# Kernel tuning notes

Measured on AMD Instinct MI355X. Metric: run time of the kernel, lower is better.

Reference implementation:

```python
import jax, jax.numpy as jnp
import numpy as np

E, K = 8, 2              # n_routed_experts, num_experts_per_tok
H, I = 2048, 1408        # hidden_size, moe_intermediate_size
IS = 2 * I               # shared experts intermediate (n_shared_experts * I)
B, S = 2, 512


def setup_inputs() -> dict:
    key = jax.random.key(0)
    ks = jax.random.split(key, 8)
    w = 0.02
    return {
        "hidden_states": jax.random.normal(ks[0], (B, S, H), jnp.float32),
        "router_w": jax.random.normal(ks[1], (E, H), jnp.float32) * w,
        "w_gate": jax.random.normal(ks[2], (E, I, H), jnp.float32) * w,
        "w_up": jax.random.normal(ks[3], (E, I, H), jnp.float32) * w,
        "w_down": jax.random.normal(ks[4], (E, H, I), jnp.float32) * w,
        "sw_gate": jax.random.normal(ks[5], (IS, H), jnp.float32) * w,
        "sw_up": jax.random.normal(ks[6], (IS, H), jnp.float32) * w,
        "sw_down": jax.random.normal(ks[7], (H, IS), jnp.float32) * w,
    }


def reference(hidden_states, router_w, w_gate, w_up, w_down, sw_gate, sw_up, sw_down):
    b, s, h = hidden_states.shape
    x = hidden_states.reshape(-1, h)                      # [T, H]
    t = x.shape[0]

    # Router: F.linear(x, gate_weight) -> softmax (fp32) -> topk (sorted)
    router_logits = x @ router_w.T                        # [T, E]
    scores = jax.nn.softmax(router_logits.astype(jnp.float32), axis=-1)
    routing_weights, selected = jax.lax.top_k(scores, K)  # [T, K]
    routing_weights = routing_weights / (routing_weights.sum(-1, keepdims=True) + 1e-6)
    routing_weights = routing_weights.astype(x.dtype)

    # Combine weights: [T, E], zero where expert not selected (exact gather/scatter math)
    cw = jnp.zeros((t, E), x.dtype).at[jnp.arange(t)[:, None], selected].add(routing_weights)

    # Per-expert SwiGLU FFN, batched over experts (grouped GEMM form)
    g = jnp.einsum('td,eid->eti', x, w_gate)              # [E, T, I]
    u = jnp.einsum('td,eid->eti', x, w_up)                # [E, T, I]
    y = jnp.einsum('eti,edi->etd', jax.nn.silu(g) * u, w_down)  # [E, T, H]
    moe_out = jnp.einsum('etd,te->td', y, cw)             # weighted combine -> [T, H]

    # Shared experts SwiGLU over all tokens
    shared = (jax.nn.silu(x @ sw_gate.T) * (x @ sw_up.T)) @ sw_down.T  # [T, H]

    final = (moe_out + shared).reshape(b, s, h)
    return final, router_logits
```

## Files before the change

### kernel.cpp

```cpp
#include <hip/hip_runtime.h>
#include <hip/hip_bf16.h>
#include <math.h>

#define T_TOK 1024
#define HDIM  2048
#define NEXP  8
#define IDIM  1408
#define ISH   2816
#define ROW_CAP 3072
#define ROWS_ALL 4096
#define MOE_TILES 24
#define NT_TOT 32

typedef __attribute__((ext_vector_type(8))) short bf16x8;
typedef __attribute__((ext_vector_type(4))) float f32x4;

static __device__ __forceinline__ unsigned short f2bf(float f) {
  __hip_bfloat16 h = __float2bfloat16(f);
  return __builtin_bit_cast(unsigned short, h);
}

__global__ __launch_bounds__(256) void router_kernel(
    const float* __restrict__ x, const float* __restrict__ rw,
    float* __restrict__ logits_out, int* __restrict__ selk, float* __restrict__ cwk)
{
  int t = blockIdx.x;
  int tid = threadIdx.x;
  float part[NEXP];
  const float* xr = x + (size_t)t * HDIM + tid * 8;
  float4 xa = *reinterpret_cast<const float4*>(xr);
  float4 xb = *reinterpret_cast<const float4*>(xr + 4);
  for (int e = 0; e < NEXP; ++e) {
    const float* wp = rw + (size_t)e * HDIM + tid * 8;
    float4 wa = *reinterpret_cast<const float4*>(wp);
    float4 wb = *reinterpret_cast<const float4*>(wp + 4);
    part[e] = xa.x*wa.x + xa.y*wa.y + xa.z*wa.z + xa.w*wa.w
            + xb.x*wb.x + xb.y*wb.y + xb.z*wb.z + xb.w*wb.w;
  }
  for (int e = 0; e < NEXP; ++e)
    for (int off = 32; off; off >>= 1)
      part[e] += __shfl_xor(part[e], off, 64);
  __shared__ float sums[4][NEXP];
  int wid = tid >> 6, lane = tid & 63;
  if (lane == 0) for (int e = 0; e < NEXP; ++e) sums[wid][e] = part[e];
  __syncthreads();
  if (tid == 0) {
    float lg[NEXP];
    for (int e = 0; e < NEXP; ++e) lg[e] = sums[0][e] + sums[1][e] + sums[2][e] + sums[3][e];
    float mx = lg[0];
    for (int e = 1; e < NEXP; ++e) mx = fmaxf(mx, lg[e]);
    float p[NEXP], s = 0.f;
    for (int e = 0; e < NEXP; ++e) { p[e] = expf(lg[e] - mx); s += p[e]; }
    for (int e = 0; e < NEXP; ++e) p[e] /= s;
    int i1 = 0;
    for (int e = 1; e < NEXP; ++e) if (lg[e] > lg[i1]) i1 = e;
    int i2 = -1;
    for (int e = 0; e < NEXP; ++e) { if (e == i1) continue; if (i2 < 0 || lg[e] > lg[i2]) i2 = e; }
    float denom = p[i1] + p[i2] + 1e-6f;
    selk[t*2] = i1; selk[t*2+1] = i2;
    cwk[t*2] = p[i1] / denom; cwk[t*2+1] = p[i2] / denom;
    for (int e = 0; e < NEXP; ++e) logits_out[t * NEXP + e] = lg[e];
  }
}

__global__ __launch_bounds__(512) void plan_kernel(
    const int* __restrict__ selk, const float* __restrict__ cwk,
    int* __restrict__ rowidx, int* __restrict__ tok_of_row,
    float* __restrict__ rowwgt, int* __restrict__ tile_tab)
{
  __shared__ int cnt[NEXP];
  __shared__ int seg[NEXP];
  int tid = threadIdx.x;
  int w = tid >> 6, lane = tid & 63;
  for (int i = tid; i < ROW_CAP; i += 512) { tok_of_row[i] = -1; rowwgt[i] = 0.f; }
  for (int i = tid; i < T_TOK; i += 512) { tok_of_row[ROW_CAP + i] = i; rowwgt[ROW_CAP + i] = 1.f; }
  int total = 0;
  for (int base = 0; base < 2 * T_TOK; base += 64) {
    unsigned long long m = __ballot(selk[base + lane] == w);
    total += __popcll(m);
  }
  if (lane == 0) cnt[w] = total;
  __syncthreads();
  if (tid == 0) {
    int s = 0;
    for (int e = 0; e < NEXP; ++e) { seg[e] = s; s += (cnt[e] + 127) & ~127; }
  }
  __syncthreads();
  int run = seg[w];
  for (int base = 0; base < 2 * T_TOK; base += 64) {
    int i = base + lane;
    bool f = selk[i] == w;
    unsigned long long m = __ballot(f);
    if (f) {
      int r = run + __popcll(m & ((1ull << lane) - 1ull));
      rowidx[i] = r;
      tok_of_row[r] = i >> 1;
      rowwgt[r] = cwk[i];
    }
    run += __popcll(m);
  }
  __syncthreads();
  if (tid < NT_TOT) {
    int e = -1, valid = 0;
    if (tid < MOE_TILES) {
      int base = tid * 128;
      for (int k = 0; k < NEXP; ++k) {
        int s0 = seg[k], s1 = s0 + ((cnt[k] + 127) & ~127);
        if (base >= s0 && base < s1) {
          e = k;
          valid = cnt[k] - (base - s0);
          if (valid > 128) valid = 128;
          if (valid < 0) valid = 0;
        }
      }
    } else { e = 0; valid = 128; }
    tile_tab[tid*2] = e;
    tile_tab[tid*2+1] = valid;
  }
}

__global__ __launch_bounds__(256) void gather_kernel(
    const float* __restrict__ x, const int* __restrict__ tok_of_row,
    unsigned short* __restrict__ xg)
{
  int r = blockIdx.x;
  int tid = threadIdx.x;
  int tok = tok_of_row[r];
  unsigned short* dst = xg + (size_t)r * HDIM + tid * 8;
  union { unsigned short us[8]; uint4 q; } p;
  if (tok < 0) {
    p.q = uint4{0, 0, 0, 0};
  } else {
    const float* src = x + (size_t)tok * HDIM + tid * 8;
    float4 a = *reinterpret_cast<const float4*>(src);
    float4 b = *reinterpret_cast<const float4*>(src + 4);
    p.us[0]=f2bf(a.x); p.us[1]=f2bf(a.y); p.us[2]=f2bf(a.z); p.us[3]=f2bf(a.w);
    p.us[4]=f2bf(b.x); p.us[5]=f2bf(b.y); p.us[6]=f2bf(b.z); p.us[7]=f2bf(b.w);
  }
  *reinterpret_cast<uint4*>(dst) = p.q;
}

__global__ __launch_bounds__(256) void wcvt_kernel(
    const float* __restrict__ s0, const float* __restrict__ s1,
    const float* __restrict__ s2, const float* __restrict__ s3,
    unsigned short* __restrict__ d0, unsigned short* __restrict__ d1,
    unsigned short* __restrict__ d2, unsigned short* __restrict__ d3,
    int b0, int b1, int b2)
{
  int b = blockIdx.x;
  const float* s; unsigned short* d; int off;
  if (b < b0)      { s = s0; d = d0; off = b; }
  else if (b < b1) { s = s1; d = d1; off = b - b0; }
  else if (b < b2) { s = s2; d = d2; off = b - b1; }
  else             { s = s3; d = d3; off = b - b2; }
  size_t idx = (size_t)off * 2048 + threadIdx.x * 8;
  float4 va = *reinterpret_cast<const float4*>(s + idx);
  float4 vb = *reinterpret_cast<const float4*>(s + idx + 4);
  union { unsigned short us[8]; uint4 q; } p;
  p.us[0]=f2bf(va.x); p.us[1]=f2bf(va.y); p.us[2]=f2bf(va.z); p.us[3]=f2bf(va.w);
  p.us[4]=f2bf(vb.x); p.us[5]=f2bf(vb.y); p.us[6]=f2bf(vb.z); p.us[7]=f2bf(vb.w);
  *reinterpret_cast<uint4*>(d + idx) = p.q;
}

static __device__ __forceinline__ void stage_t(
    const unsigned short* __restrict__ base, size_t ld, int k0,
    unsigned short* Ls, int wid, int lane)
{
  #pragma unroll
  for (int j = 0; j < 2; ++j) {
    int row = j * 64 + wid * 8 + (lane >> 3);
    int col = ((lane & 7) ^ (row & 7)) << 3;
    const unsigned short* src = base + (size_t)row * ld + k0 + col;
    unsigned short* dst = &Ls[(j * 64 + wid * 8) * 64];
    __builtin_amdgcn_global_load_lds(
        (const __attribute__((address_space(1))) void*)src,
        (__attribute__((address_space(3))) void*)dst, 16, 0, 0);
  }
}

__global__ __launch_bounds__(512) void gu_kernel(
    const unsigned short* __restrict__ xg,
    const unsigned short* __restrict__ wgb, const unsigned short* __restrict__ wub,
    const unsigned short* __restrict__ swgb, const unsigned short* __restrict__ swub,
    const float* __restrict__ rowwgt, const int* __restrict__ tile_tab,
    unsigned short* __restrict__ hg, unsigned short* __restrict__ hsh)
{
  int bid = blockIdx.x;
  int lb = (bid & 7) * 55 + (bid >> 3);
  int mt, nt;
  if (lb < MOE_TILES * 11) { mt = lb % MOE_TILES; nt = lb / MOE_TILES; }
  else { int s = lb - MOE_TILES * 11; mt = MOE_TILES + (s & 7); nt = s >> 3; }

  int e = tile_tab[mt*2], valid = tile_tab[mt*2+1];
  if (valid <= 0) return;
  bool sh = mt >= MOE_TILES;
  int m0 = mt * 128, n0 = nt * 128;
  const unsigned short *wg, *wu; unsigned short* hout; int ldo;
  if (sh) { wg = swgb; wu = swub; hout = hsh + (size_t)(m0 - ROW_CAP) * ISH; ldo = ISH; }
  else {
    size_t wo = (size_t)e * IDIM * HDIM;
    wg = wgb + wo; wu = wub + wo;
    hout = hg + (size_t)m0 * IDIM; ldo = IDIM;
  }

  __shared__ unsigned short As[128 * 64];
  __shared__ unsigned short Bg[128 * 64];
  __shared__ unsigned short Bu[128 * 64];

  int tid = threadIdx.x, wid = tid >> 6, lane = tid & 63;
  int wr = wid >> 2, wc = wid & 3;
  int fr = lane & 15, fq = lane >> 4, fq8 = fq << 3;

  f32x4 accg[4][2] = {{}};
  f32x4 accu[4][2] = {{}};

  const unsigned short* abase = xg + (size_t)m0 * HDIM;
  const unsigned short* gb = wg + (size_t)n0 * HDIM;
  const unsigned short* ub = wu + (size_t)n0 * HDIM;

  for (int k0 = 0; k0 < HDIM; k0 += 64) {
    stage_t(abase, HDIM, k0, As, wid, lane);
    stage_t(gb,    HDIM, k0, Bg, wid, lane);
    stage_t(ub,    HDIM, k0, Bu, wid, lane);
    __syncthreads();
    #pragma unroll
    for (int kk = 0; kk < 64; kk += 32) {
      bf16x8 a[4], bg[2], bu[2];
      #pragma unroll
      for (int m = 0; m < 4; ++m) {
        int row = wr * 64 + m * 16 + fr;
        a[m] = *reinterpret_cast<const bf16x8*>(&As[row * 64 + ((kk + fq8) ^ ((row & 7) << 3))]);
      }
      #pragma unroll
      for (int n = 0; n < 2; ++n) {
        int brow = wc * 32 + n * 16 + fr;
        int boff = brow * 64 + ((kk + fq8) ^ ((brow & 7) << 3));
        bg[n] = *reinterpret_cast<const bf16x8*>(&Bg[boff]);
        bu[n] = *reinterpret_cast<const bf16x8*>(&Bu[boff]);
      }
      #pragma unroll
      for (int m = 0; m < 4; ++m)
        #pragma unroll
        for (int n = 0; n < 2; ++n) {
          accg[m][n] = __builtin_amdgcn_mfma_f32_16x16x32_bf16(a[m], bg[n], accg[m][n], 0, 0, 0);
          accu[m][n] = __builtin_amdgcn_mfma_f32_16x16x32_bf16(a[m], bu[n], accu[m][n], 0, 0, 0);
        }
    }
    __syncthreads();
  }

  #pragma unroll
  for (int m = 0; m < 4; ++m)
    #pragma unroll
    for (int j = 0; j < 4; ++j) {
      int grow = wr * 64 + m * 16 + fq * 4 + j;
      float wv = rowwgt[m0 + grow];
      #pragma unroll
      for (int n = 0; n < 2; ++n) {
        float g = accg[m][n][j], u = accu[m][n][j];
        float hv = g / (1.f + __expf(-g)) * u * wv;
        hout[(size_t)grow * ldo + n0 + wc * 32 + n * 16 + fr] = f2bf(hv);
      }
    }
}

__global__ __launch_bounds__(512) void dn_kernel(
    const unsigned short* __restrict__ hg, const unsigned short* __restrict__ hsh,
    const unsigned short* __restrict__ wdb, const unsigned short* __restrict__ swdb,
    const int* __restrict__ tile_tab,
    float* __restrict__ ydn, float* __restrict__ outf)
{
  int bid = blockIdx.x;
  int lb = (bid & 7) * 64 + (bid >> 3);
  int mt, nt;
  if (lb < MOE_TILES * 16) { mt = lb % MOE_TILES; nt = lb / MOE_TILES; }
  else { int s = lb - MOE_TILES * 16; mt = MOE_TILES + (s & 7); nt = s >> 3; }

  int e = tile_tab[mt*2], valid = tile_tab[mt*2+1];
  if (valid <= 0) return;
  bool sh = mt >= MOE_TILES;
  int m0 = mt * 128, n0 = nt * 128;
  const unsigned short* abase; const unsigned short* bbase; int K; float* obase;
  if (sh) { abase = hsh + (size_t)(m0 - ROW_CAP) * ISH; K = ISH; bbase = swdb; obase = outf + (size_t)(m0 - ROW_CAP) * HDIM; }
  else { abase = hg + (size_t)m0 * IDIM; K = IDIM; bbase = wdb + (size_t)e * HDIM * IDIM; obase = ydn + (size_t)m0 * HDIM; }

  __shared__ unsigned short As[128 * 64];
  __shared__ unsigned short Bs[128 * 64];

  int tid = threadIdx.x, wid = tid >> 6, lane = tid & 63;
  int wr = wid >> 2, wc = wid & 3;
  int fr = lane & 15, fq = lane >> 4, fq8 = fq << 3;

  f32x4 acc[4][2] = {{}};

  const unsigned short* bb = bbase + (size_t)n0 * K;

  for (int k0 = 0; k0 < K; k0 += 64) {
    stage_t(abase, K, k0, As, wid, lane);
    stage_t(bb,    K, k0, Bs, wid, lane);
    __syncthreads();
    #pragma unroll
    for (int kk = 0; kk < 64; kk += 32) {
      bf16x8 a[4], b[2];
      #pragma unroll
      for (int m = 0; m < 4; ++m) {
        int row = wr * 64 + m * 16 + fr;
        a[m] = *reinterpret_cast<const bf16x8*>(&As[row * 64 + ((kk + fq8) ^ ((row & 7) << 3))]);
      }
      #pragma unroll
      for (int n = 0; n < 2; ++n) {
        int brow = wc * 32 + n * 16 + fr;
        b[n] = *reinterpret_cast<const bf16x8*>(&Bs[brow * 64 + ((kk + fq8) ^ ((brow & 7) << 3))]);
      }
      #pragma unroll
      for (int m = 0; m < 4; ++m)
        #pragma unroll
        for (int n = 0; n < 2; ++n)
          acc[m][n] = __builtin_amdgcn_mfma_f32_16x16x32_bf16(a[m], b[n], acc[m][n], 0, 0, 0);
    }
    __syncthreads();
  }
  #pragma unroll
  for (int m = 0; m < 4; ++m)
    #pragma unroll
    for (int j = 0; j < 4; ++j) {
      int grow = wr * 64 + m * 16 + fq * 4 + j;
      #pragma unroll
      for (int n = 0; n < 2; ++n)
        obase[(size_t)grow * HDIM + n0 + wc * 32 + n * 16 + fr] = acc[m][n][j];
    }
}

__global__ __launch_bounds__(256) void combine_kernel(
    const float* __restrict__ ydn, const int* __restrict__ rowidx,
    float* __restrict__ outf)
{
  int t = blockIdx.x;
  int c = threadIdx.x * 8;
  int r0 = rowidx[t*2], r1 = rowidx[t*2+1];
  const float4* a0 = reinterpret_cast<const float4*>(ydn + (size_t)r0 * HDIM + c);
  const float4* a1 = reinterpret_cast<const float4*>(ydn + (size_t)r1 * HDIM + c);
  float4* o = reinterpret_cast<float4*>(outf + (size_t)t * HDIM + c);
  float4 x0 = a0[0], x1 = a0[1], y0 = a1[0], y1 = a1[1];
  float4 o0 = o[0], o1 = o[1];
  o0.x += x0.x + y0.x; o0.y += x0.y + y0.y; o0.z += x0.z + y0.z; o0.w += x0.w + y0.w;
  o1.x += x1.x + y1.x; o1.y += x1.y + y1.y; o1.z += x1.z + y1.z; o1.w += x1.w + y1.w;
  o[0] = o0; o[1] = o1;
}

extern "C" void kernel_launch(void* const* d_in, const int* in_sizes, int n_in,
                              void* d_out, int out_size, void* d_ws, size_t ws_size,
                              hipStream_t stream) {
  const float* x      = (const float*)d_in[0];
  const float* rw     = (const float*)d_in[1];
  const float* w_gate = (const float*)d_in[2];
  const float* w_up   = (const float*)d_in[3];
  const float* w_down = (const float*)d_in[4];
  const float* sw_g   = (const float*)d_in[5];
  const float* sw_u   = (const float*)d_in[6];
  const float* sw_d   = (const float*)d_in[7];
  float* out_final  = (float*)d_out;
  float* out_logits = out_final + (size_t)T_TOK * HDIM;

  char* ws = (char*)d_ws;
  int*   selk     = (int*)(ws + 0);
  float* cwk      = (float*)(ws + 8192);
  int*   rowidx   = (int*)(ws + 16384);
  int*   tokrow   = (int*)(ws + 24576);
  float* rowwgt   = (float*)(ws + 40960);
  int*   tile_tab = (int*)(ws + 57344);
  size_t off = 65536;
  unsigned short* xg  = (unsigned short*)(ws + off);  off += (size_t)ROWS_ALL * HDIM * 2;
  unsigned short* hg  = (unsigned short*)(ws + off);  off += (size_t)ROW_CAP * IDIM * 2;
  unsigned short* hsh = (unsigned short*)(ws + off);  off += (size_t)T_TOK * ISH * 2;
  float* ydn          = (float*)(ws + off);           off += (size_t)ROW_CAP * HDIM * 4;
  unsigned short* wbuf = (unsigned short*)(ws + off);
  unsigned short* wgb  = wbuf;
  unsigned short* wub  = wgb + (size_t)NEXP * IDIM * HDIM;
  unsigned short* swgb = wub + (size_t)NEXP * IDIM * HDIM;
  unsigned short* swub = swgb + (size_t)ISH * HDIM;
  unsigned short* wdb  = wbuf;
  unsigned short* swdb = wdb + (size_t)NEXP * HDIM * IDIM;

  router_kernel<<<T_TOK, 256, 0, stream>>>(x, rw, out_logits, selk, cwk);
  plan_kernel<<<1, 512, 0, stream>>>(selk, cwk, rowidx, tokrow, rowwgt, tile_tab);
  gather_kernel<<<ROWS_ALL, 256, 0, stream>>>(x, tokrow, xg);

  wcvt_kernel<<<28160, 256, 0, stream>>>(
      w_gate, w_up, sw_g, sw_u, wgb, wub, swgb, swub, 11264, 22528, 25344);

  gu_kernel<<<440, 512, 0, stream>>>(
      xg, wgb, wub, swgb, swub, rowwgt, tile_tab, hg, hsh);

  wcvt_kernel<<<14080, 256, 0, stream>>>(
      w_down, sw_d, sw_d, sw_d, wdb, swdb, swdb, swdb, 11264, 14080, 14080);

  dn_kernel<<<512, 512, 0, stream>>>(
      hg, hsh, wdb, swdb, tile_tab, ydn, out_final);
  combine_kernel<<<T_TOK, 256, 0, stream>>>(ydn, rowidx, out_final);
}
```

Measured before the change: 288.2 us.

## Double-buffer LDS K-loop and interleave gate/up weights into one GEMM

The gate and up weight rows are converted into an interleaved layout (16 gate rows then 16 up rows), so gu_kernel runs as a single 128x128 GEMM whose two N-halves are gate and up. This halves accumulators and LDS per block and doubles the grid. Both the gu and down kernels now double-buffer the LDS tiles with async global_load_lds prefetch of the next K-slice, using a vmcnt wait plus raw barriers in place of two syncthreads per iteration. The risk is correctness of the hand-counted vmcnt and of the barrier placement that guards buffer reuse.

New measurement: 262.4 us. 9.0% less time.

```diff
diff --git a/kernel.cpp b/kernel.cpp
--- a/kernel.cpp
+++ b/kernel.cpp
@@ -11,6 +11,7 @@
 #define ROWS_ALL 4096
 #define MOE_TILES 24
 #define NT_TOT 32
+#define ATILE (128*64)
 
 typedef __attribute__((ext_vector_type(8))) short bf16x8;
 typedef __attribute__((ext_vector_type(4))) float f32x4;
@@ -19,6 +20,17 @@
   __hip_bfloat16 h = __float2bfloat16(f);
   return __builtin_bit_cast(unsigned short, h);
 }
+
+#define PIPE_WAIT(N) do { \
+    asm volatile("s_waitcnt vmcnt(" #N ")" ::: "memory"); \
+    __builtin_amdgcn_s_barrier(); \
+    __builtin_amdgcn_sched_barrier(0); \
+  } while (0)
+
+#define RAW_BAR() do { \
+    __builtin_amdgcn_s_barrier(); \
+    __builtin_amdgcn_sched_barrier(0); \
+  } while (0)
 
 __global__ __launch_bounds__(256) void router_kernel(
     const float* __restrict__ x, const float* __restrict__ rw,
@@ -140,20 +152,56 @@
   *reinterpret_cast<uint4*>(dst) = p.q;
 }
 
-__global__ __launch_bounds__(256) void wcvt_kernel(
-    const float* __restrict__ s0, const float* __restrict__ s1,
-    const float* __restrict__ s2, const float* __restrict__ s3,
-    unsigned short* __restrict__ d0, unsigned short* __restrict__ d1,
-    unsigned short* __restrict__ d2, unsigned short* __restrict__ d3,
-    int b0, int b1, int b2)
+static __device__ __forceinline__ void cvt_row(
+    const float* __restrict__ src, unsigned short* __restrict__ dst, int tid)
+{
+  size_t idx = (size_t)tid * 8;
+  float4 va = *reinterpret_cast<const float4*>(src + idx);
+  float4 vb = *reinterpret_cast<const float4*>(src + idx + 4);
+  union { unsigned short us[8]; uint4 q; } p;
+  p.us[0]=f2bf(va.x); p.us[1]=f2bf(va.y); p.us[2]=f2bf(va.z); p.us[3]=f2bf(va.w);
+  p.us[4]=f2bf(vb.x); p.us[5]=f2bf(vb.y); p.us[6]=f2bf(vb.z); p.us[7]=f2bf(vb.w);
+  *reinterpret_cast<uint4*>(dst + idx) = p.q;
+}
+
+__global__ __launch_bounds__(256) void wcvt_gu_kernel(
+    const float* __restrict__ wg, const float* __restrict__ wu,
+    const float* __restrict__ sg, const float* __restrict__ su,
+    unsigned short* __restrict__ dmoe, unsigned short* __restrict__ dsh)
 {
   int b = blockIdx.x;
-  const float* s; unsigned short* d; int off;
-  if (b < b0)      { s = s0; d = d0; off = b; }
-  else if (b < b1) { s = s1; d = d1; off = b - b0; }
-  else if (b < b2) { s = s2; d = d2; off = b - b1; }
-  else             { s = s3; d = d3; off = b - b2; }
-  size_t idx = (size_t)off * 2048 + threadIdx.x * 8;
+  const float* src; unsigned short* dst; size_t drow;
+  if (b < NEXP * IDIM) {
+    int e = b / IDIM, i = b - e * IDIM;
+    src = wg + (size_t)b * HDIM; dst = dmoe;
+    drow = (size_t)e * 2 * IDIM + ((i >> 4) << 5) + (i & 15);
+  } else if (b < 2 * NEXP * IDIM) {
+    int bb = b - NEXP * IDIM;
+    int e = bb / IDIM, i = bb - e * IDIM;
+    src = wu + (size_t)bb * HDIM; dst = dmoe;
+    drow = (size_t)e * 2 * IDIM + ((i >> 4) << 5) + 16 + (i & 15);
+  } else if (b < 2 * NEXP * IDIM + ISH) {
+    int i = b - 2 * NEXP * IDIM;
+    src = sg + (size_t)i * HDIM; dst = dsh;
+    drow = ((size_t)(i >> 4) << 5) + (i & 15);
+  } else {
+    int i = b - 2 * NEXP * IDIM - ISH;
+    src = su + (size_t)i * HDIM; dst = dsh;
+    drow = ((size_t)(i >> 4) << 5) + 16 + (i & 15);
+  }
+  cvt_row(src, dst + drow * HDIM, threadIdx.x);
+}
+
+__global__ __launch_bounds__(256) void wcvt_dn_kernel(
+    const float* __restrict__ wd, const float* __restrict__ swd,
+    unsigned short* __restrict__ dmoe, unsigned short* __restrict__ dsh,
+    int nchunks_moe)
+{
+  int b = blockIdx.x;
+  const float* s; unsigned short* d; size_t off;
+  if (b < nchunks_moe) { s = wd; d = dmoe; off = (size_t)b * 2048; }
+  else { s = swd; d = dsh; off = (size_t)(b - nchunks_moe) * 2048; }
+  size_t idx = off + threadIdx.x * 8;
   float4 va = *reinterpret_cast<const float4*>(s + idx);
   float4 vb = *reinterpret_cast<const float4*>(s + idx + 4);
   union { unsigned short us[8]; uint4 q; } p;
@@ -180,87 +228,86 @@
 
 __global__ __launch_bounds__(512) void gu_kernel(
     const unsigned short* __restrict__ xg,
-    const unsigned short* __restrict__ wgb, const unsigned short* __restrict__ wub,
-    const unsigned short* __restrict__ swgb, const unsigned short* __restrict__ swub,
+    const unsigned short* __restrict__ wgub, const unsigned short* __restrict__ swgub,
     const float* __restrict__ rowwgt, const int* __restrict__ tile_tab,
     unsigned short* __restrict__ hg, unsigned short* __restrict__ hsh)
 {
   int bid = blockIdx.x;
-  int lb = (bid & 7) * 55 + (bid >> 3);
+  int lb = (bid & 7) * 110 + (bid >> 3);
   int mt, nt;
-  if (lb < MOE_TILES * 11) { mt = lb % MOE_TILES; nt = lb / MOE_TILES; }
-  else { int s = lb - MOE_TILES * 11; mt = MOE_TILES + (s & 7); nt = s >> 3; }
+  if (lb < MOE_TILES * 22) { mt = lb % MOE_TILES; nt = lb / MOE_TILES; }
+  else { int s = lb - MOE_TILES * 22; mt = MOE_TILES + (s & 7); nt = s >> 3; }
 
   int e = tile_tab[mt*2], valid = tile_tab[mt*2+1];
   if (valid <= 0) return;
   bool sh = mt >= MOE_TILES;
-  int m0 = mt * 128, n0 = nt * 128;
-  const unsigned short *wg, *wu; unsigned short* hout; int ldo;
-  if (sh) { wg = swgb; wu = swub; hout = hsh + (size_t)(m0 - ROW_CAP) * ISH; ldo = ISH; }
+  int m0 = mt * 128;
+  const unsigned short* wb; unsigned short* hout; int ldo;
+  if (sh) { wb = swgub; hout = hsh + (size_t)(m0 - ROW_CAP) * ISH; ldo = ISH; }
   else {
-    size_t wo = (size_t)e * IDIM * HDIM;
-    wg = wgb + wo; wu = wub + wo;
+    wb = wgub + (size_t)e * 2 * IDIM * HDIM;
     hout = hg + (size_t)m0 * IDIM; ldo = IDIM;
   }
 
-  __shared__ unsigned short As[128 * 64];
-  __shared__ unsigned short Bg[128 * 64];
-  __shared__ unsigned short Bu[128 * 64];
+  __shared__ unsigned short As[2 * ATILE];
+  __shared__ unsigned short Bs[2 * ATILE];
 
   int tid = threadIdx.x, wid = tid >> 6, lane = tid & 63;
   int wr = wid >> 2, wc = wid & 3;
   int fr = lane & 15, fq = lane >> 4, fq8 = fq << 3;
 
-  f32x4 accg[4][2] = {{}};
-  f32x4 accu[4][2] = {{}};
+  f32x4 acc[4][2] = {{}};
 
   const unsigned short* abase = xg + (size_t)m0 * HDIM;
-  const unsigned short* gb = wg + (size_t)n0 * HDIM;
-  const unsigned short* ub = wu + (size_t)n0 * HDIM;
-
-  for (int k0 = 0; k0 < HDIM; k0 += 64) {
-    stage_t(abase, HDIM, k0, As, wid, lane);
-    stage_t(gb,    HDIM, k0, Bg, wid, lane);
-    stage_t(ub,    HDIM, k0, Bu, wid, lane);
-    __syncthreads();
+  const unsigned short* bbase = wb + (size_t)(nt * 128) * HDIM;
+
+  stage_t(abase, HDIM, 0, As, wid, lane);
+  stage_t(bbase, HDIM, 0, Bs, wid, lane);
+
+  const int NK = HDIM / 64;
+  for (int t = 0; t < NK; ++t) {
+    int cur = t & 1;
+    if (t + 1 < NK) {
+      stage_t(abase, HDIM, (t + 1) * 64, As + (cur ^ 1) * ATILE, wid, lane);
+      stage_t(bbase, HDIM, (t + 1) * 64, Bs + (cur ^ 1) * ATILE, wid, lane);
+      PIPE_WAIT(4);
+    } else {
+      PIPE_WAIT(0);
+    }
+    const unsigned short* Ab = As + cur * ATILE;
+    const unsigned short* Bb = Bs + cur * ATILE;
     #pragma unroll
     for (int kk = 0; kk < 64; kk += 32) {
-      bf16x8 a[4], bg[2], bu[2];
+      bf16x8 a[4], b[2];
       #pragma unroll
       for (int m = 0; m < 4; ++m) {
         int row = wr * 64 + m * 16 + fr;
-        a[m] = *reinterpret_cast<const bf16x8*>(&As[row * 64 + ((kk + fq8) ^ ((row & 7) << 3))]);
+        a[m] = *reinterpret_cast<const bf16x8*>(&Ab[row * 64 + ((kk + fq8) ^ ((row & 7) << 3))]);
       }
       #pragma unroll
       for (int n = 0; n < 2; ++n) {
         int brow = wc * 32 + n * 16 + fr;
-        int boff = brow * 64 + ((kk + fq8) ^ ((brow & 7) << 3));
-        bg[n] = *reinterpret_cast<const bf16x8*>(&Bg[boff]);
-        bu[n] = *reinterpret_cast<const bf16x8*>(&Bu[boff]);
+        b[n] = *reinterpret_cast<const bf16x8*>(&Bb[brow * 64 + ((kk + fq8) ^ ((brow & 7) << 3))]);
       }
       #pragma unroll
       for (int m = 0; m < 4; ++m)
         #pragma unroll
-        for (int n = 0; n < 2; ++n) {
-          accg[m][n] = __builtin_amdgcn_mfma_f32_16x16x32_bf16(a[m], bg[n], accg[m][n], 0, 0, 0);
-          accu[m][n] = __builtin_amdgcn_mfma_f32_16x16x32_bf16(a[m], bu[n], accu[m][n], 0, 0, 0);
-        }
-    }
-    __syncthreads();
-  }
-
+        for (int n = 0; n < 2; ++n)
+          acc[m][n] = __builtin_amdgcn_mfma_f32_16x16x32_bf16(a[m], b[n], acc[m][n], 0, 0, 0);
+    }
+    RAW_BAR();
+  }
+
+  int icol = nt * 64 + wc * 16 + fr;
   #pragma unroll
   for (int m = 0; m < 4; ++m)
     #pragma unroll
     for (int j = 0; j < 4; ++j) {
       int grow = wr * 64 + m * 16 + fq * 4 + j;
       float wv = rowwgt[m0 + grow];
-      #pragma unroll
-      for (int n = 0; n < 2; ++n) {
-        float g = accg[m][n][j], u = accu[m][n][j];
-        float hv = g / (1.f + __expf(-g)) * u * wv;
-        hout[(size_t)grow * ldo + n0 + wc * 32 + n * 16 + fr] = f2bf(hv);
-      }
+      float g = acc[m][0][j], u = acc[m][1][j];
+      float hv = g / (1.f + __expf(-g)) * u * wv;
+      hout[(size_t)grow * ldo + icol] = f2bf(hv);
     }
 }
 
@@ -284,8 +331,8 @@
   if (sh) { abase = hsh + (size_t)(m0 - ROW_CAP) * ISH; K = ISH; bbase = swdb; obase = outf + (size_t)(m0 - ROW_CAP) * HDIM; }
   else { abase = hg + (size_t)m0 * IDIM; K = IDIM; bbase = wdb + (size_t)e * HDIM * IDIM; obase = ydn + (size_t)m0 * HDIM; }
 
-  __shared__ unsigned short As[128 * 64];
-  __shared__ unsigned short Bs[128 * 64];
+  __shared__ unsigned short As[2 * ATILE];
+  __shared__ unsigned short Bs[2 * ATILE];
 
   int tid = threadIdx.x, wid = tid >> 6, lane = tid & 63;
   int wr = wid >> 2, wc = wid & 3;
@@ -295,22 +342,33 @@
 
   const unsigned short* bb = bbase + (size_t)n0 * K;
 
-  for (int k0 = 0; k0 < K; k0 += 64) {
-    stage_t(abase, K, k0, As, wid, lane);
-    stage_t(bb,    K, k0, Bs, wid, lane);
-    __syncthreads();
+  stage_t(abase, K, 0, As, wid, lane);
+  stage_t(bb,    K, 0, Bs, wid, lane);
+
+  const int NK = K / 64;
+  for (int t = 0; t < NK; ++t) {
+    int cur = t & 1;
+    if (t + 1 < NK) {
+      stage_t(abase, K, (t + 1) * 64, As + (cur ^ 1) * ATILE, wid, lane);
+      stage_t(bb,    K, (t + 1) * 64, Bs + (cur ^ 1) * ATILE, wid, lane);
+      PIPE_WAIT(4);
+    } else {
+      PIPE_WAIT(0);
+    }
+    const unsigned short* Ab = As + cur * ATILE;
+    const unsigned short* Bb = Bs + cur * ATILE;
     #pragma unroll
     for (int kk = 0; kk < 64; kk += 32) {
       bf16x8 a[4], b[2];
       #pragma unroll
       for (int m = 0; m < 4; ++m) {
         int row = wr * 64 + m * 16 + fr;
-        a[m] = *reinterpret_cast<const bf16x8*>(&As[row * 64 + ((kk + fq8) ^ ((row & 7) << 3))]);
+        a[m] = *reinterpret_cast<const bf16x8*>(&Ab[row * 64 + ((kk + fq8) ^ ((row & 7) << 3))]);
       }
       #pragma unroll
       for (int n = 0; n < 2; ++n) {
         int brow = wc * 32 + n * 16 + fr;
-        b[n] = *reinterpret_cast<const bf16x8*>(&Bs[brow * 64 + ((kk + fq8) ^ ((brow & 7) << 3))]);
+        b[n] = *reinterpret_cast<const bf16x8*>(&Bb[brow * 64 + ((kk + fq8) ^ ((brow & 7) << 3))]);
       }
       #pragma unroll
       for (int m = 0; m < 4; ++m)
@@ -318,7 +376,7 @@
         for (int n = 0; n < 2; ++n)
           acc[m][n] = __builtin_amdgcn_mfma_f32_16x16x32_bf16(a[m], b[n], acc[m][n], 0, 0, 0);
     }
-    __syncthreads();
+    RAW_BAR();
   }
   #pragma unroll
   for (int m = 0; m < 4; ++m)
@@ -374,28 +432,22 @@
   unsigned short* hg  = (unsigned short*)(ws + off);  off += (size_t)ROW_CAP * IDIM * 2;
   unsigned short* hsh = (unsigned short*)(ws + off);  off += (size_t)T_TOK * ISH * 2;
   float* ydn          = (float*)(ws + off);           off += (size_t)ROW_CAP * HDIM * 4;
-  unsigned short* wbuf = (unsigned short*)(ws + off);
-  unsigned short* wgb  = wbuf;
-  unsigned short* wub  = wgb + (size_t)NEXP * IDIM * HDIM;
-  unsigned short* swgb = wub + (size_t)NEXP * IDIM * HDIM;
-  unsigned short* swub = swgb + (size_t)ISH * HDIM;
-  unsigned short* wdb  = wbuf;
-  unsigned short* swdb = wdb + (size_t)NEXP * HDIM * IDIM;
+  unsigned short* wbuf  = (unsigned short*)(ws + off);
+  unsigned short* wgub  = wbuf;
+  unsigned short* swgub = wgub + (size_t)NEXP * 2 * IDIM * HDIM;
+  unsigned short* wdb   = wbuf;
+  unsigned short* swdb  = wdb + (size_t)NEXP * HDIM * IDIM;
 
   router_kernel<<<T_TOK, 256, 0, stream>>>(x, rw, out_logits, selk, cwk);
   plan_kernel<<<1, 512, 0, stream>>>(selk, cwk, rowidx, tokrow, rowwgt, tile_tab);
   gather_kernel<<<ROWS_ALL, 256, 0, stream>>>(x, tokrow, xg);
 
-  wcvt_kernel<<<28160, 256, 0, stream>>>(
-      w_gate, w_up, sw_g, sw_u, wgb, wub, swgb, swub, 11264, 22528, 25344);
-
-  gu_kernel<<<440, 512, 0, stream>>>(
-      xg, wgb, wub, swgb, swub, rowwgt, tile_tab, hg, hsh);
-
-  wcvt_kernel<<<14080, 256, 0, stream>>>(
-      w_down, sw_d, sw_d, sw_d, wdb, swdb, swdb, swdb, 11264, 14080, 14080);
-
-  dn_kernel<<<512, 512, 0, stream>>>(
-      hg, hsh, wdb, swdb, tile_tab, ydn, out_final);
+  wcvt_gu_kernel<<<28160, 256, 0, stream>>>(w_gate, w_up, sw_g, sw_u, wgub, swgub);
+
+  gu_kernel<<<880, 512, 0, stream>>>(xg, wgub, swgub, rowwgt, tile_tab, hg, hsh);
+
+  wcvt_dn_kernel<<<14080, 256, 0, stream>>>(w_down, sw_d, wdb, swdb, 11264);
+
+  dn_kernel<<<512, 512, 0, stream>>>(hg, hsh, wdb, swdb, tile_tab, ydn, out_final);
   combine_kernel<<<T_TOK, 256, 0, stream>>>(ydn, rowidx, out_final);
 }
```
